# Performance work log

Hardware: AMD Instinct MI355X
Metric: run time of the kernel (lower is better)

The kernel has to match this reference:

```python
import jax, jax.numpy as jnp
import numpy as np

C = 343.0                      # wave speed
OMEGA = 2.0 * np.pi * 1000.0   # angular frequency
K2 = (C / OMEGA) ** 2          # coefficient on u in the (as-written) residual

N_POINTS = 262144
HIDDEN = 256


def _mlp_point(p, W1, b1, W2, b2, W3, b3, W4, b4):
    # p: (3,) -> scalar u(x,y,z); tanh MLP stand-in for model_estimation
    h = jnp.tanh(p @ W1 + b1)
    h = jnp.tanh(h @ W2 + b2)
    h = jnp.tanh(h @ W3 + b3)
    return (h @ W4 + b4)[0]


def setup_inputs() -> dict:
    key = jax.random.key(0)
    ks = jax.random.split(key, 5)

    def init_w(k, fan_in, fan_out):
        return jax.random.normal(k, (fan_in, fan_out), dtype=jnp.float32) / np.sqrt(fan_in).astype(np.float32)

    inputs = jax.random.normal(ks[0], (N_POINTS, 3), dtype=jnp.float32)
    W1 = init_w(ks[1], 3, HIDDEN)
    W2 = init_w(ks[2], HIDDEN, HIDDEN)
    W3 = init_w(ks[3], HIDDEN, HIDDEN)
    W4 = init_w(ks[4], HIDDEN, 1)
    z = lambda n: jnp.zeros((n,), dtype=jnp.float32)
    return {
        "inputs": inputs,
        "W1": W1, "b1": z(HIDDEN),
        "W2": W2, "b2": z(HIDDEN),
        "W3": W3, "b3": z(HIDDEN),
        "W4": W4, "b4": z(1),
    }


def reference(inputs, W1, b1, W2, b2, W3, b3, W4, b4):
    # Per-point scalar field u(p); Laplacian = trace of the 3x3 Hessian.
    def u_point(p):
        return _mlp_point(p, W1, b1, W2, b2, W3, b3, W4, b4)

    u = jax.vmap(u_point)(inputs)                       # [N]
    hess = jax.vmap(jax.hessian(u_point))(inputs)       # [N, 3, 3]
    laplace_u = hess[:, 0, 0] + hess[:, 1, 1] + hess[:, 2, 2]  # [N]

    pde_residual = laplace_u + K2 * u
    return jnp.mean(jnp.abs(pde_residual) ** 2)
```

## Files before the change

### kernel.cpp

```cpp
#include <hip/hip_runtime.h>
#include <math.h>

#define HID 256
#define PTS 16
#define NSTR 5
#define ROWS (NSTR*PTS)
#define PITCH 272
#define XS(r,c) ((c) ^ (((r)&1)<<3))

typedef __fp16  fp16x2 __attribute__((ext_vector_type(2)));
typedef _Float16 half8  __attribute__((ext_vector_type(8)));
typedef float   floatx4 __attribute__((ext_vector_type(4)));

constexpr double PI_D = 3.14159265358979323846;
constexpr float K2F = (float)((343.0/(2.0*PI_D*1000.0))*(343.0/(2.0*PI_D*1000.0)));

union H2U { fp16x2 h; unsigned int u; };
__device__ __forceinline__ unsigned int pk(float a, float b) {
  H2U t; t.h = __builtin_amdgcn_cvt_pkrtz(a, b); return t.u;
}

__device__ __forceinline__ float tanh_fast(float z) {
  float e = __builtin_amdgcn_exp2f(z * 2.8853900817779268f);
  return 1.0f - 2.0f * __builtin_amdgcn_rcpf(e + 1.0f);
}

__global__ void pack_kernel(const float* __restrict__ W2, const float* __restrict__ W3,
                            const float* __restrict__ W1,
                            _Float16* __restrict__ out, float* __restrict__ wsq) {
  if (blockIdx.x == 64) {
    int n = threadIdx.x;
    float w0 = W1[0*HID + n], w1 = W1[1*HID + n], w2 = W1[2*HID + n];
    wsq[n] = fmaf(w0, w0, fmaf(w1, w1, w2*w2));
    return;
  }
  int t = blockIdx.x * blockDim.x + threadIdx.x;
  int l    = t >> 13;
  int rem  = t & 8191;
  int kc   = rem >> 10;
  int nt   = (rem >> 6) & 15;
  int lane = rem & 63;
  const float* W = l ? W3 : W2;
  int k0 = kc*32 + ((lane >> 4) << 3);
  int n  = (nt >> 2)*64 + (lane & 15)*4 + (nt & 3);
  _Float16* o = out + (size_t)t * 8;
  #pragma unroll
  for (int j = 0; j < 8; ++j)
    o[j] = (_Float16)W[(size_t)(k0 + j)*HID + n];
}

__global__ __launch_bounds__(256, 3) void helm_kernel(
    const float* __restrict__ inputs,
    const float* __restrict__ W1, const float* __restrict__ b1,
    const float* __restrict__ b2, const float* __restrict__ b3,
    const float* __restrict__ W4, const float* __restrict__ b4,
    const _Float16* __restrict__ Wpack,
    const float* __restrict__ wsqv,
    float* __restrict__ part)
{
  __shared__ __align__(16) _Float16 X[ROWS][PITCH];

  const int tid  = threadIdx.x;
  const int lane = tid & 63;
  const int wave = tid >> 6;
  const int m    = lane & 15;
  const int q    = lane >> 4;

  const int pbase = blockIdx.x * PTS;

  {
    const int p  = tid >> 4;
    const int c0 = (tid & 15) * 16;
    const float x0 = inputs[(size_t)(pbase + p)*3 + 0];
    const float x1 = inputs[(size_t)(pbase + p)*3 + 1];
    const float x2 = inputs[(size_t)(pbase + p)*3 + 2];
    #pragma unroll
    for (int ch = 0; ch < 2; ++ch) {
      float v[NSTR][8];
      #pragma unroll
      for (int jj = 0; jj < 2; ++jj) {
        const int n = c0 + ch*8 + jj*4;
        floatx4 w0 = *(const floatx4*)&W1[0*HID + n];
        floatx4 w1 = *(const floatx4*)&W1[1*HID + n];
        floatx4 w2 = *(const floatx4*)&W1[2*HID + n];
        floatx4 bn = *(const floatx4*)&b1[n];
        floatx4 ws = *(const floatx4*)&wsqv[n];
        #pragma unroll
        for (int e = 0; e < 4; ++e) {
          float z  = fmaf(x2, w2[e], fmaf(x1, w1[e], fmaf(x0, w0[e], bn[e])));
          float a  = tanh_fast(z);
          float dd = 1.0f - a*a;
          v[0][jj*4+e] = a;
          v[1][jj*4+e] = dd*w0[e];
          v[2][jj*4+e] = dd*w1[e];
          v[3][jj*4+e] = dd*w2[e];
          v[4][jj*4+e] = -2.0f*a*dd*ws[e];
        }
      }
      #pragma unroll
      for (int s = 0; s < NSTR; ++s) {
        uint4 u;
        u.x = pk(v[s][0], v[s][1]); u.y = pk(v[s][2], v[s][3]);
        u.z = pk(v[s][4], v[s][5]); u.w = pk(v[s][6], v[s][7]);
        *(uint4*)&X[s*PTS + p][XS(p, c0 + ch*8)] = u;
      }
    }
  }
  __syncthreads();

  const int colbase = wave*64 + m*4;

  auto kloop = [&](const _Float16* __restrict__ Wp, floatx4 (&acc)[NSTR][4]) {
    const _Float16* wb = Wp + (((size_t)(wave*4)*64 + lane) << 3);
    half8 bnxt[4];
    #pragma unroll
    for (int c = 0; c < 4; ++c)
      bnxt[c] = *(const half8*)(wb + c*512);
    #pragma unroll
    for (int kc = 0; kc < 8; ++kc) {
      half8 bcur[4];
      #pragma unroll
      for (int c = 0; c < 4; ++c) bcur[c] = bnxt[c];
      if (kc < 7) {
        #pragma unroll
        for (int c = 0; c < 4; ++c)
          bnxt[c] = *(const half8*)(wb + (size_t)(kc+1)*8192 + c*512);
      }
      half8 acur = *(const half8*)(&X[0*PTS + m][XS(m, kc*32 + q*8)]);
      #pragma unroll
      for (int s = 0; s < NSTR; ++s) {
        half8 anxt;
        if (s + 1 < NSTR)
          anxt = *(const half8*)(&X[(s+1)*PTS + m][XS(m, kc*32 + q*8)]);
        #pragma unroll
        for (int c = 0; c < 4; ++c)
          acc[s][c] = __builtin_amdgcn_mfma_f32_16x16x32_f16(acur, bcur[c], acc[s][c], 0, 0, 0);
        if (s + 1 < NSTR) acur = anxt;
      }
    }
  };

  {
    floatx4 acc[NSTR][4];
    #pragma unroll
    for (int s = 0; s < NSTR; ++s)
      #pragma unroll
      for (int c = 0; c < 4; ++c)
        acc[s][c] = (floatx4){0.0f, 0.0f, 0.0f, 0.0f};
    kloop(Wpack, acc);
    __syncthreads();

    floatx4 bv = *(const floatx4*)&b2[colbase];
    #pragma unroll
    for (int r = 0; r < 4; ++r) {
      const int p = q*4 + r;
      float va[4], vg0[4], vg1[4], vg2[4], vT[4];
      #pragma unroll
      for (int c = 0; c < 4; ++c) {
        float z  = acc[0][c][r] + bv[c];
        float a  = tanh_fast(z);
        float dd = 1.0f - a*a;
        float z0 = acc[1][c][r], z1 = acc[2][c][r], z2 = acc[3][c][r];
        float zpp = acc[4][c][r];
        float s2 = fmaf(z0, z0, fmaf(z1, z1, z2*z2));
        va[c]  = a;
        vg0[c] = dd*z0; vg1[c] = dd*z1; vg2[c] = dd*z2;
        vT[c]  = fmaf(dd, zpp, -2.0f*a*dd*s2);
      }
      const int cs = XS(p, colbase);
      uint2 u;
      u.x = pk(va[0],va[1]);   u.y = pk(va[2],va[3]);   *(uint2*)&X[0*PTS + p][cs] = u;
      u.x = pk(vg0[0],vg0[1]); u.y = pk(vg0[2],vg0[3]); *(uint2*)&X[1*PTS + p][cs] = u;
      u.x = pk(vg1[0],vg1[1]); u.y = pk(vg1[2],vg1[3]); *(uint2*)&X[2*PTS + p][cs] = u;
      u.x = pk(vg2[0],vg2[1]); u.y = pk(vg2[2],vg2[3]); *(uint2*)&X[3*PTS + p][cs] = u;
      u.x = pk(vT[0],vT[1]);   u.y = pk(vT[2],vT[3]);   *(uint2*)&X[4*PTS + p][cs] = u;
    }
    __syncthreads();
  }

  {
    floatx4 acc[NSTR][4];
    #pragma unroll
    for (int s = 0; s < NSTR; ++s)
      #pragma unroll
      for (int c = 0; c < 4; ++c)
        acc[s][c] = (floatx4){0.0f, 0.0f, 0.0f, 0.0f};
    kloop(Wpack + 65536, acc);
    __syncthreads();

    floatx4 bv = *(const floatx4*)&b3[colbase];
    floatx4 w4 = *(const floatx4*)&W4[colbase];
    float su[4] = {0,0,0,0}, st[4] = {0,0,0,0};
    #pragma unroll
    for (int r = 0; r < 4; ++r)
      #pragma unroll
      for (int c = 0; c < 4; ++c) {
        float z  = acc[0][c][r] + bv[c];
        float a  = tanh_fast(z);
        float dd = 1.0f - a*a;
        float z0 = acc[1][c][r], z1 = acc[2][c][r], z2 = acc[3][c][r];
        float zpp = acc[4][c][r];
        float s2 = fmaf(z0, z0, fmaf(z1, z1, z2*z2));
        float T  = fmaf(dd, zpp, -2.0f*a*dd*s2);
        su[r] = fmaf(a, w4[c], su[r]);
        st[r] = fmaf(T, w4[c], st[r]);
      }

    #pragma unroll
    for (int off = 8; off >= 1; off >>= 1)
      #pragma unroll
      for (int r = 0; r < 4; ++r) {
        su[r] += __shfl_down(su[r], off);
        st[r] += __shfl_down(st[r], off);
      }
    float* S = (float*)X;
    if (m == 0) {
      #pragma unroll
      for (int r = 0; r < 4; ++r) {
        S[(q*4 + r)*8 + wave]     = su[r];
        S[(q*4 + r)*8 + 4 + wave] = st[r];
      }
    }
  }
  __syncthreads();

  if (wave == 0) {
    const float* S = (const float*)X;
    int pidx = lane >> 2, w = lane & 3;
    float suc = S[pidx*8 + w];
    float stc = S[pidx*8 + 4 + w];
    suc += __shfl_down(suc, 1); suc += __shfl_down(suc, 2);
    stc += __shfl_down(stc, 1); stc += __shfl_down(stc, 2);
    float sq = 0.0f;
    if ((lane & 3) == 0) {
      float u   = suc + b4[0];
      float res = fmaf(K2F, u, stc);
      sq = res * res;
    }
    sq += __shfl_down(sq, 4); sq += __shfl_down(sq, 8);
    sq += __shfl_down(sq, 16); sq += __shfl_down(sq, 32);
    if (lane == 0) part[blockIdx.x] = sq;
  }
}

__global__ void reduce_kernel(const float* __restrict__ part, float* __restrict__ out,
                              int nblk, float scale) {
  float s = 0.0f;
  for (int i = threadIdx.x; i < (nblk >> 2); i += 256) {
    floatx4 v = *(const floatx4*)&part[i << 2];
    s += (v[0] + v[1]) + (v[2] + v[3]);
  }
  #pragma unroll
  for (int off = 32; off; off >>= 1) s += __shfl_down(s, off);
  __shared__ float sm[4];
  if ((threadIdx.x & 63) == 0) sm[threadIdx.x >> 6] = s;
  __syncthreads();
  if (threadIdx.x == 0) out[0] = ((sm[0] + sm[1]) + (sm[2] + sm[3])) * scale;
}

extern "C" void kernel_launch(void* const* d_in, const int* in_sizes, int n_in,
                              void* d_out, int out_size, void* d_ws, size_t ws_size,
                              hipStream_t stream) {
  const float* inputs = (const float*)d_in[0];
  const float* W1 = (const float*)d_in[1];
  const float* b1 = (const float*)d_in[2];
  const float* W2 = (const float*)d_in[3];
  const float* b2 = (const float*)d_in[4];
  const float* W3 = (const float*)d_in[5];
  const float* b3 = (const float*)d_in[6];
  const float* W4 = (const float*)d_in[7];
  const float* b4 = (const float*)d_in[8];
  float* out = (float*)d_out;

  _Float16* wp   = (_Float16*)d_ws;
  float*    part = (float*)((char*)d_ws + 2*65536*2);
  float*    wsq  = (float*)((char*)d_ws + 2*65536*2 + 65536);

  int N    = in_sizes[0] / 3;
  int nblk = N / PTS;

  pack_kernel<<<65, 256, 0, stream>>>(W2, W3, W1, wp, wsq);
  helm_kernel<<<nblk, 256, 0, stream>>>(inputs, W1, b1, b2, b3, W4, b4, wp, wsq, part);
  reduce_kernel<<<1, 256, 0, stream>>>(part, out, nblk, 1.0f / (float)N);
}
```

Baseline: 433.4 us.

## Split GEMM columns into halves and overlap tanh epilogue with second-half MFMAs

After: 514.8 us. 18.8% more time.

```diff
diff --git a/kernel.cpp b/kernel.cpp
--- a/kernel.cpp
+++ b/kernel.cpp
@@ -6,7 +6,6 @@
 #define NSTR 5
 #define ROWS (NSTR*PTS)
 #define PITCH 272
-#define XS(r,c) ((c) ^ (((r)&1)<<3))
 
 typedef __fp16  fp16x2 __attribute__((ext_vector_type(2)));
 typedef _Float16 half8  __attribute__((ext_vector_type(8)));
@@ -102,117 +101,206 @@
         uint4 u;
         u.x = pk(v[s][0], v[s][1]); u.y = pk(v[s][2], v[s][3]);
         u.z = pk(v[s][4], v[s][5]); u.w = pk(v[s][6], v[s][7]);
-        *(uint4*)&X[s*PTS + p][XS(p, c0 + ch*8)] = u;
+        *(uint4*)&X[s*PTS + p][c0 + ch*8] = u;
       }
     }
   }
   __syncthreads();
 
   const int colbase = wave*64 + m*4;
-
-  auto kloop = [&](const _Float16* __restrict__ Wp, floatx4 (&acc)[NSTR][4]) {
-    const _Float16* wb = Wp + (((size_t)(wave*4)*64 + lane) << 3);
-    half8 bnxt[4];
-    #pragma unroll
-    for (int c = 0; c < 4; ++c)
-      bnxt[c] = *(const half8*)(wb + c*512);
+  const _Float16* wb2 = Wpack + (((size_t)(wave*4)*64 + lane) << 3);
+  const _Float16* wb3 = wb2 + 65536;
+
+  auto kloop_half = [&](const _Float16* __restrict__ wb, int off,
+                        floatx4 (&acc)[NSTR][2]) {
+    #pragma unroll
+    for (int s = 0; s < NSTR; ++s)
+      #pragma unroll
+      for (int c = 0; c < 2; ++c)
+        acc[s][c] = (floatx4){0.0f, 0.0f, 0.0f, 0.0f};
     #pragma unroll
     for (int kc = 0; kc < 8; ++kc) {
-      half8 bcur[4];
-      #pragma unroll
-      for (int c = 0; c < 4; ++c) bcur[c] = bnxt[c];
-      if (kc < 7) {
-        #pragma unroll
-        for (int c = 0; c < 4; ++c)
-          bnxt[c] = *(const half8*)(wb + (size_t)(kc+1)*8192 + c*512);
-      }
-      half8 acur = *(const half8*)(&X[0*PTS + m][XS(m, kc*32 + q*8)]);
-      #pragma unroll
-      for (int s = 0; s < NSTR; ++s) {
-        half8 anxt;
-        if (s + 1 < NSTR)
-          anxt = *(const half8*)(&X[(s+1)*PTS + m][XS(m, kc*32 + q*8)]);
-        #pragma unroll
-        for (int c = 0; c < 4; ++c)
-          acc[s][c] = __builtin_amdgcn_mfma_f32_16x16x32_f16(acur, bcur[c], acc[s][c], 0, 0, 0);
-        if (s + 1 < NSTR) acur = anxt;
-      }
+      half8 bfrag[2];
+      #pragma unroll
+      for (int c = 0; c < 2; ++c)
+        bfrag[c] = *(const half8*)(wb + (size_t)kc*8192 + (off + c)*512);
+      half8 afrag[NSTR];
+      #pragma unroll
+      for (int s = 0; s < NSTR; ++s)
+        afrag[s] = *(const half8*)(&X[s*PTS + m][kc*32 + q*8]);
+      #pragma unroll
+      for (int s = 0; s < NSTR; ++s)
+        #pragma unroll
+        for (int c = 0; c < 2; ++c)
+          acc[s][c] = __builtin_amdgcn_mfma_f32_16x16x32_f16(afrag[s], bfrag[c], acc[s][c], 0, 0, 0);
     }
   };
 
-  {
-    floatx4 acc[NSTR][4];
+  auto combine_pair = [&](floatx4 (&acc2)[NSTR][2], float bv0, float bv1,
+                          unsigned int (&o)[NSTR]) {
+    float t0[NSTR], t1[NSTR];
+    #pragma unroll
+    for (int c2 = 0; c2 < 2; ++c2) {
+      float z  = acc2[0][c2][0] + (c2 ? bv1 : bv0);
+      (void)z;
+      t0[0] = t0[0];
+    }
+    (void)t0; (void)t1; (void)o;
+  };
+  (void)combine_pair;
+
+  floatx4 acc01[NSTR][2], acc23[NSTR][2];
+  unsigned int bufA[4][5];
+
+  kloop_half(wb2, 0, acc01);
+
+  {
+    const float bv0 = b2[colbase + 0];
+    const float bv1 = b2[colbase + 1];
     #pragma unroll
     for (int s = 0; s < NSTR; ++s)
       #pragma unroll
-      for (int c = 0; c < 4; ++c)
-        acc[s][c] = (floatx4){0.0f, 0.0f, 0.0f, 0.0f};
-    kloop(Wpack, acc);
-    __syncthreads();
-
-    floatx4 bv = *(const floatx4*)&b2[colbase];
+      for (int c = 0; c < 2; ++c)
+        acc23[s][c] = (floatx4){0.0f, 0.0f, 0.0f, 0.0f};
+    #pragma unroll
+    for (int kc = 0; kc < 8; ++kc) {
+      half8 bfrag[2];
+      #pragma unroll
+      for (int c = 0; c < 2; ++c)
+        bfrag[c] = *(const half8*)(wb2 + (size_t)kc*8192 + (2 + c)*512);
+      half8 afrag[NSTR];
+      #pragma unroll
+      for (int s = 0; s < NSTR; ++s)
+        afrag[s] = *(const half8*)(&X[s*PTS + m][kc*32 + q*8]);
+      #pragma unroll
+      for (int s = 0; s < NSTR; ++s)
+        #pragma unroll
+        for (int c = 0; c < 2; ++c)
+          acc23[s][c] = __builtin_amdgcn_mfma_f32_16x16x32_f16(afrag[s], bfrag[c], acc23[s][c], 0, 0, 0);
+      if ((kc & 1) == 0) {
+        const int r = kc >> 1;
+        float o0[NSTR], o1[NSTR];
+        #pragma unroll
+        for (int c2 = 0; c2 < 2; ++c2) {
+          float z  = acc01[0][c2][r] + (c2 ? bv1 : bv0);
+          float a  = tanh_fast(z);
+          float dd = 1.0f - a*a;
+          float z0 = acc01[1][c2][r], z1 = acc01[2][c2][r], z2 = acc01[3][c2][r];
+          float zpp = acc01[4][c2][r];
+          float s2 = fmaf(z0, z0, fmaf(z1, z1, z2*z2));
+          float* o = c2 ? o1 : o0;
+          o[0] = a;
+          o[1] = dd*z0; o[2] = dd*z1; o[3] = dd*z2;
+          o[4] = fmaf(dd, zpp, -2.0f*a*dd*s2);
+        }
+        #pragma unroll
+        for (int s = 0; s < NSTR; ++s)
+          bufA[r][s] = pk(o0[s], o1[s]);
+      }
+    }
+  }
+  __syncthreads();
+
+  {
+    const float bv2 = b2[colbase + 2];
+    const float bv3v = b2[colbase + 3];
     #pragma unroll
     for (int r = 0; r < 4; ++r) {
       const int p = q*4 + r;
-      float va[4], vg0[4], vg1[4], vg2[4], vT[4];
-      #pragma unroll
-      for (int c = 0; c < 4; ++c) {
-        float z  = acc[0][c][r] + bv[c];
+      #pragma unroll
+      for (int s = 0; s < NSTR; ++s)
+        *(unsigned int*)&X[s*PTS + p][colbase] = bufA[r][s];
+      float o0[NSTR], o1[NSTR];
+      #pragma unroll
+      for (int c2 = 0; c2 < 2; ++c2) {
+        float z  = acc23[0][c2][r] + (c2 ? bv3v : bv2);
         float a  = tanh_fast(z);
         float dd = 1.0f - a*a;
-        float z0 = acc[1][c][r], z1 = acc[2][c][r], z2 = acc[3][c][r];
-        float zpp = acc[4][c][r];
+        float z0 = acc23[1][c2][r], z1 = acc23[2][c2][r], z2 = acc23[3][c2][r];
+        float zpp = acc23[4][c2][r];
         float s2 = fmaf(z0, z0, fmaf(z1, z1, z2*z2));
-        va[c]  = a;
-        vg0[c] = dd*z0; vg1[c] = dd*z1; vg2[c] = dd*z2;
-        vT[c]  = fmaf(dd, zpp, -2.0f*a*dd*s2);
-      }
-      const int cs = XS(p, colbase);
-      uint2 u;
-      u.x = pk(va[0],va[1]);   u.y = pk(va[2],va[3]);   *(uint2*)&X[0*PTS + p][cs] = u;
-      u.x = pk(vg0[0],vg0[1]); u.y = pk(vg0[2],vg0[3]); *(uint2*)&X[1*PTS + p][cs] = u;
-      u.x = pk(vg1[0],vg1[1]); u.y = pk(vg1[2],vg1[3]); *(uint2*)&X[2*PTS + p][cs] = u;
-      u.x = pk(vg2[0],vg2[1]); u.y = pk(vg2[2],vg2[3]); *(uint2*)&X[3*PTS + p][cs] = u;
-      u.x = pk(vT[0],vT[1]);   u.y = pk(vT[2],vT[3]);   *(uint2*)&X[4*PTS + p][cs] = u;
-    }
-    __syncthreads();
-  }
-
-  {
-    floatx4 acc[NSTR][4];
+        float* o = c2 ? o1 : o0;
+        o[0] = a;
+        o[1] = dd*z0; o[2] = dd*z1; o[3] = dd*z2;
+        o[4] = fmaf(dd, zpp, -2.0f*a*dd*s2);
+      }
+      #pragma unroll
+      for (int s = 0; s < NSTR; ++s)
+        *(unsigned int*)&X[s*PTS + p][colbase + 2] = pk(o0[s], o1[s]);
+    }
+  }
+  __syncthreads();
+
+  float su[4] = {0,0,0,0}, st[4] = {0,0,0,0};
+
+  kloop_half(wb3, 0, acc01);
+
+  {
+    const float bva[2] = { b3[colbase + 0], b3[colbase + 1] };
+    const float w4a[2] = { W4[colbase + 0], W4[colbase + 1] };
     #pragma unroll
     for (int s = 0; s < NSTR; ++s)
       #pragma unroll
-      for (int c = 0; c < 4; ++c)
-        acc[s][c] = (floatx4){0.0f, 0.0f, 0.0f, 0.0f};
-    kloop(Wpack + 65536, acc);
-    __syncthreads();
-
-    floatx4 bv = *(const floatx4*)&b3[colbase];
-    floatx4 w4 = *(const floatx4*)&W4[colbase];
-    float su[4] = {0,0,0,0}, st[4] = {0,0,0,0};
-    #pragma unroll
-    for (int r = 0; r < 4; ++r)
-      #pragma unroll
-      for (int c = 0; c < 4; ++c) {
-        float z  = acc[0][c][r] + bv[c];
+      for (int c = 0; c < 2; ++c)
+        acc23[s][c] = (floatx4){0.0f, 0.0f, 0.0f, 0.0f};
+    #pragma unroll
+    for (int kc = 0; kc < 8; ++kc) {
+      half8 bfrag[2];
+      #pragma unroll
+      for (int c = 0; c < 2; ++c)
+        bfrag[c] = *(const half8*)(wb3 + (size_t)kc*8192 + (2 + c)*512);
+      half8 afrag[NSTR];
+      #pragma unroll
+      for (int s = 0; s < NSTR; ++s)
+        afrag[s] = *(const half8*)(&X[s*PTS + m][kc*32 + q*8]);
+      #pragma unroll
+      for (int s = 0; s < NSTR; ++s)
+        #pragma unroll
+        for (int c = 0; c < 2; ++c)
+          acc23[s][c] = __builtin_amdgcn_mfma_f32_16x16x32_f16(afrag[s], bfrag[c], acc23[s][c], 0, 0, 0);
+      {
+        const int r = kc >> 1, c2 = kc & 1;
+        float z  = acc01[0][c2][r] + bva[c2];
         float a  = tanh_fast(z);
         float dd = 1.0f - a*a;
-        float z0 = acc[1][c][r], z1 = acc[2][c][r], z2 = acc[3][c][r];
-        float zpp = acc[4][c][r];
+        float z0 = acc01[1][c2][r], z1 = acc01[2][c2][r], z2 = acc01[3][c2][r];
+        float zpp = acc01[4][c2][r];
         float s2 = fmaf(z0, z0, fmaf(z1, z1, z2*z2));
         float T  = fmaf(dd, zpp, -2.0f*a*dd*s2);
-        su[r] = fmaf(a, w4[c], su[r]);
-        st[r] = fmaf(T, w4[c], st[r]);
-      }
-
-    #pragma unroll
-    for (int off = 8; off >= 1; off >>= 1)
-      #pragma unroll
-      for (int r = 0; r < 4; ++r) {
-        su[r] += __shfl_down(su[r], off);
-        st[r] += __shfl_down(st[r], off);
-      }
+        su[r] = fmaf(a, w4a[c2], su[r]);
+        st[r] = fmaf(T, w4a[c2], st[r]);
+      }
+    }
+  }
+
+  {
+    const float bvb[2] = { b3[colbase + 2], b3[colbase + 3] };
+    const float w4b[2] = { W4[colbase + 2], W4[colbase + 3] };
+    #pragma unroll
+    for (int r = 0; r < 4; ++r)
+      #pragma unroll
+      for (int c2 = 0; c2 < 2; ++c2) {
+        float z  = acc23[0][c2][r] + bvb[c2];
+        float a  = tanh_fast(z);
+        float dd = 1.0f - a*a;
+        float z0 = acc23[1][c2][r], z1 = acc23[2][c2][r], z2 = acc23[3][c2][r];
+        float zpp = acc23[4][c2][r];
+        float s2 = fmaf(z0, z0, fmaf(z1, z1, z2*z2));
+        float T  = fmaf(dd, zpp, -2.0f*a*dd*s2);
+        su[r] = fmaf(a, w4b[c2], su[r]);
+        st[r] = fmaf(T, w4b[c2], st[r]);
+      }
+  }
+
+  #pragma unroll
+  for (int off = 8; off >= 1; off >>= 1)
+    #pragma unroll
+    for (int r = 0; r < 4; ++r) {
+      su[r] += __shfl_down(su[r], off);
+      st[r] += __shfl_down(st[r], off);
+    }
+  __syncthreads();
+  {
     float* S = (float*)X;
     if (m == 0) {
       #pragma unroll
```
